# Kernel tuning notes

Hardware: AMD Instinct MI355X
Metric: run time of the kernel (lower is better)

## Reference

```python
import jax, jax.numpy as jnp
import numpy as np
from jax.scipy.special import gammaln

N_L, N_Q, D_IN, D_CTX, H, MAX_AGENT = 256, 65536, 384, 192, 64, 6
STD2 = 0.1
VAR2 = STD2 * STD2
LOG_VAR2 = float(np.log(VAR2))
TEMP = 1.0


def _linear_init(k, out_dim, in_dim):
    k1, k2 = jax.random.split(k)
    s = 1.0 / np.sqrt(in_dim)
    w = jax.random.uniform(k1, (out_dim, in_dim), minval=-s, maxval=s, dtype=jnp.float32)
    b = jax.random.uniform(k2, (out_dim,), minval=-s, maxval=s, dtype=jnp.float32)
    return w, b


def setup_inputs() -> dict:
    key = jax.random.key(0)
    ks = jax.random.split(key, 12)
    fc1_w, fc1_b = _linear_init(ks[0], H, D_IN)
    fc21_w, fc21_b = _linear_init(ks[1], H, H)
    fc22_w, fc22_b = _linear_init(ks[2], H, H)
    fc3_w, fc3_b = _linear_init(ks[3], H, H)
    fc4_w, fc4_b = _linear_init(ks[4], D_IN, H)
    ctx_w, ctx_b = _linear_init(ks[5], H, D_CTX)
    llms = jax.random.normal(ks[6], (N_L, D_IN), dtype=jnp.float32)
    contexts = jax.random.normal(ks[7], (N_Q, D_CTX), dtype=jnp.float32)
    agent_num_int = jax.random.randint(ks[8], (N_Q, 1), 1, MAX_AGENT + 1, dtype=jnp.int32)
    agent_num_float = agent_num_int.astype(jnp.float32)
    noise_eps = jax.random.normal(ks[9], (N_L, H), dtype=jnp.float32)   # VAE reparameterize eps
    rand_u = jax.random.uniform(ks[10], (MAX_AGENT, N_Q, 1), dtype=jnp.float32)  # per-step uniforms
    return dict(llms=llms, contexts=contexts, agent_num_int=agent_num_int,
                agent_num_float=agent_num_float,
                fc1_w=fc1_w, fc1_b=fc1_b, fc21_w=fc21_w, fc21_b=fc21_b,
                fc22_w=fc22_w, fc22_b=fc22_b, fc3_w=fc3_w, fc3_b=fc3_b,
                fc4_w=fc4_w, fc4_b=fc4_b, ctx_w=ctx_w, ctx_b=ctx_b,
                noise_eps=noise_eps, rand_u=rand_u)


def _l2norm(x):
    n = jnp.sqrt(jnp.sum(x * x, axis=1, keepdims=True))
    return x / jnp.maximum(n, 1e-12)


def reference(llms, contexts, agent_num_int, agent_num_float,
              fc1_w, fc1_b, fc21_w, fc21_b, fc22_w, fc22_b,
              fc3_w, fc3_b, fc4_w, fc4_b, ctx_w, ctx_b, noise_eps, rand_u):
    # ---- VAE encode / reparameterize / decode ----
    h = jax.nn.relu(llms @ fc1_w.T + fc1_b)
    mu = h @ fc21_w.T + fc21_b
    log_var = h @ fc22_w.T + fc22_b
    std = jnp.exp(0.5 * log_var) * STD2
    z = mu + noise_eps * std
    h2 = jax.nn.relu(z @ fc3_w.T + fc3_b)
    x_hat = h2 @ fc4_w.T + fc4_b
    mse = jnp.mean((x_hat - llms) ** 2)
    kld = -0.5 * jnp.mean(1.0 - LOG_VAR2 + log_var - (mu ** 2 + jnp.exp(log_var)) / VAR2)
    vae_loss = mse + kld

    # ---- embeddings and routing scores ----
    llm_emb = _l2norm(z)                                   # [N_l, H]
    ctx_emb = _l2norm(contexts @ ctx_w.T + ctx_b)          # [N_q, H]
    scores = jax.nn.softmax((ctx_emb @ llm_emb.T) / TEMP, axis=1)  # [N_q, N_l]
    scores_cumsum = jnp.cumsum(scores, axis=1)

    # ---- vectorized max_agent-step categorical sampling ----
    # sel[i, q] = first llm where cumsum > u (inverse-CDF sampling), for step i
    sel = jnp.argmax(scores_cumsum[None, :, :] > rand_u, axis=2)          # [A, N_q]
    steps = jnp.arange(1, rand_u.shape[0] + 1, dtype=agent_num_int.dtype)
    mask = (agent_num_int[None, :, 0] >= steps[:, None]).astype(scores.dtype)  # [A, N_q]
    rows = jnp.broadcast_to(jnp.arange(scores.shape[0])[None, :], sel.shape)
    selected_llm = jnp.zeros_like(scores).at[rows, sel].add(mask)          # [N_q, N_l]

    log_probs = (gammaln(agent_num_float + 1.0)
                 - jnp.sum(gammaln(selected_llm + 1.0), axis=1, keepdims=True)
                 + jnp.sum(selected_llm * jnp.log(scores), axis=1, keepdims=True))
    return selected_llm, log_probs, vae_loss
```

## Files before the change

kernel.cpp:

```cpp
#include <hip/hip_runtime.h>
#include <hip/hip_bf16.h>

#define N_L 256
#define N_Q 65536
#define D_IN 384
#define D_CTX 192
#define HDIM 64
#define MAXA 6

__device__ __forceinline__ void fma4(float& acc, const float4& w, const float4& v) {
    acc = fmaf(w.x, v.x, acc);
    acc = fmaf(w.y, v.y, acc);
    acc = fmaf(w.z, v.z, acc);
    acc = fmaf(w.w, v.w, acc);
}

__device__ __forceinline__ float lgfact(int n) {
    return (n <= 1) ? 0.0f :
           (n == 2) ? 0.6931471805599453f :
           (n == 3) ? 1.7917594692280550f :
           (n == 4) ? 3.1780538303479458f :
           (n == 5) ? 4.7874917427820460f :
                      6.5792512120101010f;
}

__global__ __launch_bounds__(64) void vae_kernel(
    const float* __restrict__ llms, const float* __restrict__ ctx_w,
    const float* __restrict__ fc1_w, const float* __restrict__ fc1_b,
    const float* __restrict__ fc21_w, const float* __restrict__ fc21_b,
    const float* __restrict__ fc22_w, const float* __restrict__ fc22_b,
    const float* __restrict__ fc3_w, const float* __restrict__ fc3_b,
    const float* __restrict__ fc4_w, const float* __restrict__ fc4_b,
    const float* __restrict__ eps,
    float* __restrict__ ctx_wP, float* __restrict__ embT,
    float* __restrict__ mse_row, float* __restrict__ kld_row)
{
    __shared__ __align__(16) float xs[D_IN];
    __shared__ __align__(16) float hs[HDIM];
    __shared__ __align__(16) float zs[HDIM];
    __shared__ __align__(16) float h2s[HDIM];
    const int r = blockIdx.x;
    const int j = threadIdx.x;

    {
        int f = r * 64 + j;
        if (f < D_CTX * HDIM) {
            int p = f >> 2, rr = f & 3;
            int jc = p & 63, k4 = p >> 6;
            ctx_wP[f] = ctx_w[jc * D_CTX + k4 * 4 + rr];
        }
    }

    for (int k = j; k < D_IN; k += 64) xs[k] = llms[r * D_IN + k];
    __syncthreads();

    float acc = fc1_b[j];
    {
        const float4* wr = (const float4*)(fc1_w + (size_t)j * D_IN);
        const float4* xr = (const float4*)xs;
        #pragma unroll 8
        for (int k4 = 0; k4 < D_IN / 4; ++k4) { fma4(acc, wr[k4], xr[k4]); }
    }
    float h = fmaxf(acc, 0.0f);
    hs[j] = h;
    __syncthreads();

    float mu = fc21_b[j], lv = fc22_b[j];
    {
        const float4* w1 = (const float4*)(fc21_w + (size_t)j * HDIM);
        const float4* w2 = (const float4*)(fc22_w + (size_t)j * HDIM);
        const float4* hr = (const float4*)hs;
        #pragma unroll
        for (int k4 = 0; k4 < HDIM / 4; ++k4) {
            float4 hh = hr[k4];
            fma4(mu, w1[k4], hh);
            fma4(lv, w2[k4], hh);
        }
    }
    float stdv = expf(0.5f * lv) * 0.1f;
    float z = fmaf(eps[r * HDIM + j], stdv, mu);

    float elv = expf(lv);
    float kt = (1.0f - (-4.60517018598809136f)) + lv - (mu * mu + elv) / 0.01f;
    float ks = kt;
    #pragma unroll
    for (int o = 32; o; o >>= 1) ks += __shfl_xor(ks, o);

    float zsq = z * z;
    #pragma unroll
    for (int o = 32; o; o >>= 1) zsq += __shfl_xor(zsq, o);
    float nrm = fmaxf(sqrtf(zsq), 1e-12f);
    embT[j * N_L + r] = z / nrm;
    zs[j] = z;
    __syncthreads();

    float a3 = fc3_b[j];
    {
        const float4* w3 = (const float4*)(fc3_w + (size_t)j * HDIM);
        const float4* zr = (const float4*)zs;
        #pragma unroll
        for (int k4 = 0; k4 < HDIM / 4; ++k4) { fma4(a3, w3[k4], zr[k4]); }
    }
    float h2 = fmaxf(a3, 0.0f);
    h2s[j] = h2;
    __syncthreads();

    float ms = 0.0f;
    const float4* h2r = (const float4*)h2s;
    #pragma unroll
    for (int m = 0; m < 6; ++m) {
        int o = j + 64 * m;
        float a4 = fc4_b[o];
        const float4* w4 = (const float4*)(fc4_w + (size_t)o * HDIM);
        #pragma unroll
        for (int k4 = 0; k4 < HDIM / 4; ++k4) { fma4(a4, w4[k4], h2r[k4]); }
        float d = a4 - xs[o];
        ms = fmaf(d, d, ms);
    }
    #pragma unroll
    for (int o = 32; o; o >>= 1) ms += __shfl_xor(ms, o);
    if (j == 0) { mse_row[r] = ms; kld_row[r] = ks; }
}

__global__ __launch_bounds__(256) void route_kernel(
    const float* __restrict__ contexts, const float* __restrict__ ctx_wP, const float* __restrict__ ctx_b,
    const float* __restrict__ embT, const int* __restrict__ agent_num, const float* __restrict__ rand_u,
    const float* __restrict__ mse_row, const float* __restrict__ kld_row,
    float* __restrict__ out_sel, float* __restrict__ out_lp, float* __restrict__ out_loss)
{
    __shared__ __align__(16) float lds[4][1600];

    const int tid = threadIdx.x;
    const int lane = tid & 63;
    const int widx = tid >> 6;
    const int l0 = lane << 2;

    const int g = blockIdx.x * 4 + widx;
    const int q0 = __builtin_amdgcn_readfirstlane(g << 3);
    float* myl = lds[widx];

    {
        float4* xls = (float4*)myl;
        const float4* cbase = (const float4*)contexts + (size_t)q0 * (D_CTX / 4);
        #pragma unroll
        for (int it = 0; it < 6; ++it) {
            int f = lane + it * 64;
            xls[f] = cbase[f];
        }
        if (lane < 48)
            myl[1536 + lane] = rand_u[(lane >> 3) * N_Q + q0 + (lane & 7)];
    }

    if (g == 0) {
        int rr = lane * 4;
        float ms = mse_row[rr] + mse_row[rr + 1] + mse_row[rr + 2] + mse_row[rr + 3];
        float ks = kld_row[rr] + kld_row[rr + 1] + kld_row[rr + 2] + kld_row[rr + 3];
        #pragma unroll
        for (int o = 32; o; o >>= 1) { ms += __shfl_xor(ms, o); ks += __shfl_xor(ks, o); }
        if (lane == 0) out_loss[0] = ms / 98304.0f - 0.5f * (ks / 16384.0f);
    }

    int Aq[8];
    #pragma unroll
    for (int q = 0; q < 8; ++q)
        Aq[q] = __builtin_amdgcn_readfirstlane(agent_num[q0 + q]);

    const float bj = ctx_b[lane];
    float e[8];
    #pragma unroll
    for (int q = 0; q < 8; ++q) e[q] = bj;
    {
        const float4* wp = (const float4*)ctx_wP;
        const float4* xls = (const float4*)myl;
        #pragma unroll 2
        for (int k4 = 0; k4 < D_CTX / 4; ++k4) {
            float4 w = wp[k4 * HDIM + lane];
            #pragma unroll
            for (int q = 0; q < 8; ++q) {
                float4 xv = xls[q * 48 + k4];
                e[q] = fmaf(w.x, xv.x, e[q]);
                e[q] = fmaf(w.y, xv.y, e[q]);
                e[q] = fmaf(w.z, xv.z, e[q]);
                e[q] = fmaf(w.w, xv.w, e[q]);
            }
        }
    }
    {
        float s[8];
        #pragma unroll
        for (int q = 0; q < 8; ++q) s[q] = e[q] * e[q];
        #pragma unroll
        for (int o = 32; o; o >>= 1)
            #pragma unroll
            for (int q = 0; q < 8; ++q) s[q] += __shfl_xor(s[q], o);
        #pragma unroll
        for (int q = 0; q < 8; ++q) {
            e[q] *= 1.0f / fmaxf(sqrtf(s[q]), 1e-12f);
            myl[q * HDIM + lane] = e[q];
        }
    }

    float4 P[8];
    #pragma unroll
    for (int q = 0; q < 8; ++q) P[q] = make_float4(0.f, 0.f, 0.f, 0.f);

    #pragma unroll 2
    for (int j4 = 0; j4 < HDIM / 4; ++j4) {
        float4 M0 = *(const float4*)(embT + (size_t)(j4 * 4 + 0) * N_L + l0);
        float4 M1 = *(const float4*)(embT + (size_t)(j4 * 4 + 1) * N_L + l0);
        float4 M2 = *(const float4*)(embT + (size_t)(j4 * 4 + 2) * N_L + l0);
        float4 M3 = *(const float4*)(embT + (size_t)(j4 * 4 + 3) * N_L + l0);
        #pragma unroll
        for (int q = 0; q < 8; ++q) {
            float4 ev = *(const float4*)(myl + q * HDIM + j4 * 4);
            P[q].x = fmaf(M0.x, ev.x, P[q].x); P[q].x = fmaf(M1.x, ev.y, P[q].x);
            P[q].x = fmaf(M2.x, ev.z, P[q].x); P[q].x = fmaf(M3.x, ev.w, P[q].x);
            P[q].y = fmaf(M0.y, ev.x, P[q].y); P[q].y = fmaf(M1.y, ev.y, P[q].y);
            P[q].y = fmaf(M2.y, ev.z, P[q].y); P[q].y = fmaf(M3.y, ev.w, P[q].y);
            P[q].z = fmaf(M0.z, ev.x, P[q].z); P[q].z = fmaf(M1.z, ev.y, P[q].z);
            P[q].z = fmaf(M2.z, ev.z, P[q].z); P[q].z = fmaf(M3.z, ev.w, P[q].z);
            P[q].w = fmaf(M0.w, ev.x, P[q].w); P[q].w = fmaf(M1.w, ev.y, P[q].w);
            P[q].w = fmaf(M2.w, ev.z, P[q].w); P[q].w = fmaf(M3.w, ev.w, P[q].w);
        }
    }

    {
        float m[8], s[8];
        #pragma unroll
        for (int k = 0; k < 8; ++k) m[k] = fmaxf(fmaxf(P[k].x, P[k].y), fmaxf(P[k].z, P[k].w));
        #pragma unroll
        for (int o = 32; o; o >>= 1)
            #pragma unroll
            for (int k = 0; k < 8; ++k) m[k] = fmaxf(m[k], __shfl_xor(m[k], o));
        #pragma unroll
        for (int k = 0; k < 8; ++k) {
            P[k].x = expf(P[k].x - m[k]); P[k].y = expf(P[k].y - m[k]);
            P[k].z = expf(P[k].z - m[k]); P[k].w = expf(P[k].w - m[k]);
            s[k] = P[k].x + P[k].y + P[k].z + P[k].w;
        }
        #pragma unroll
        for (int o = 32; o; o >>= 1)
            #pragma unroll
            for (int k = 0; k < 8; ++k) s[k] += __shfl_xor(s[k], o);
        #pragma unroll
        for (int k = 0; k < 8; ++k) {
            float inv = 1.0f / s[k];
            P[k].x *= inv; P[k].y *= inv; P[k].z *= inv; P[k].w *= inv;
        }
    }

    float c0[8], c1[8], c2[8], c3[8];
    {
        float p3[8], t[8];
        #pragma unroll
        for (int k = 0; k < 8; ++k) {
            c0[k] = P[k].x; c1[k] = c0[k] + P[k].y; c2[k] = c1[k] + P[k].z; p3[k] = c2[k] + P[k].w;
            t[k] = p3[k];
        }
        #pragma unroll
        for (int o = 1; o < 64; o <<= 1)
            #pragma unroll
            for (int k = 0; k < 8; ++k) { float v = __shfl_up(t[k], o); if (lane >= o) t[k] += v; }
        #pragma unroll
        for (int k = 0; k < 8; ++k) {
            float base = t[k] - p3[k];
            c0[k] += base; c1[k] += base; c2[k] += base; c3[k] = p3[k] + base;
        }
    }

    unsigned nib[8] = {0, 0, 0, 0, 0, 0, 0, 0};
    #pragma unroll
    for (int i = 0; i < MAXA; ++i) {
        #pragma unroll
        for (int k = 0; k < 8; ++k) {
            if (i < Aq[k]) {
                float u = myl[1536 + i * 8 + k];
                unsigned long long b0 = __ballot(c0[k] <= u);
                unsigned long long b1 = __ballot(c1[k] <= u);
                unsigned long long b2 = __ballot(c2[k] <= u);
                unsigned long long b3 = __ballot(c3[k] <= u);
                int loc = __popcll(b0) + __popcll(b1) + __popcll(b2) + __popcll(b3);
                int sel = (loc >= N_L) ? 0 : loc;
                unsigned d = (unsigned)(sel - l0);
                if (d < 4u) nib[k] += 1u << (4 * d);
            }
        }
    }

    float term[8];
    #pragma unroll
    for (int k = 0; k < 8; ++k) {
        int n0 = nib[k] & 15, n1 = (nib[k] >> 4) & 15, n2 = (nib[k] >> 8) & 15, n3 = (nib[k] >> 12) & 15;
        float4 rowv = make_float4((float)n0, (float)n1, (float)n2, (float)n3);
        *(((float4*)(out_sel + (size_t)(q0 + k) * N_L)) + lane) = rowv;
        float tm = 0.0f;
        if (n0) tm += (float)n0 * logf(P[k].x) - lgfact(n0);
        if (n1) tm += (float)n1 * logf(P[k].y) - lgfact(n1);
        if (n2) tm += (float)n2 * logf(P[k].z) - lgfact(n2);
        if (n3) tm += (float)n3 * logf(P[k].w) - lgfact(n3);
        term[k] = tm;
    }
    #pragma unroll
    for (int o = 32; o; o >>= 1)
        #pragma unroll
        for (int k = 0; k < 8; ++k) term[k] += __shfl_xor(term[k], o);

    if (lane < 8) {
        float rr = term[0];
        int Aa = Aq[0];
        #pragma unroll
        for (int k = 1; k < 8; ++k) {
            if (lane == k) { rr = term[k]; Aa = Aq[k]; }
        }
        out_lp[q0 + lane] = lgfact(Aa) + rr;
    }
}

extern "C" void kernel_launch(void* const* d_in, const int* in_sizes, int n_in,
                              void* d_out, int out_size, void* d_ws, size_t ws_size,
                              hipStream_t stream) {
    const float* llms      = (const float*)d_in[0];
    const float* contexts  = (const float*)d_in[1];
    const int*   agent_i   = (const int*)  d_in[2];
    const float* fc1_w  = (const float*)d_in[4];  const float* fc1_b  = (const float*)d_in[5];
    const float* fc21_w = (const float*)d_in[6];  const float* fc21_b = (const float*)d_in[7];
    const float* fc22_w = (const float*)d_in[8];  const float* fc22_b = (const float*)d_in[9];
    const float* fc3_w  = (const float*)d_in[10]; const float* fc3_b  = (const float*)d_in[11];
    const float* fc4_w  = (const float*)d_in[12]; const float* fc4_b  = (const float*)d_in[13];
    const float* ctx_w  = (const float*)d_in[14]; const float* ctx_b  = (const float*)d_in[15];
    const float* noise  = (const float*)d_in[16]; const float* rand_u = (const float*)d_in[17];

    float* out      = (float*)d_out;
    float* out_sel  = out;
    float* out_lp   = out + (size_t)N_Q * N_L;
    float* out_loss = out_lp + N_Q;

    float* ctx_wP   = (float*)d_ws;
    float* embT     = ctx_wP + D_CTX * HDIM;
    float* mse_row  = embT + HDIM * N_L;
    float* kld_row  = mse_row + N_L;

    vae_kernel<<<N_L, 64, 0, stream>>>(llms, ctx_w, fc1_w, fc1_b, fc21_w, fc21_b, fc22_w, fc22_b,
                                       fc3_w, fc3_b, fc4_w, fc4_b, noise,
                                       ctx_wP, embT, mse_row, kld_row);
    route_kernel<<<2048, 256, 0, stream>>>(contexts, ctx_wP, ctx_b, embT, agent_i, rand_u,
                                           mse_row, kld_row, out_sel, out_lp, out_loss);
}
```

Measured before the change: 228.6 us.

## Move VAE decoder into extra route-kernel blocks and halve route LDS

Splits the VAE kernel so the small serial pre-kernel only runs the encoder. The fc3/fc4 decoder and MSE run as 64 extra blocks appended to the route kernel, with an atomic accumulator and a last-arriver counter to finalize the loss. The route kernel also stages contexts into LDS in two halves, which cuts per-wave LDS from 1600 to 832 floats, and sets launch_bounds to 8 blocks so occupancy can rise. The risks are atomic nondeterminism in the MSE sum and added register pressure from the occupancy hint.

```diff
diff --git a/kernel.cpp b/kernel.cpp
--- a/kernel.cpp
+++ b/kernel.cpp
@@ -7,6 +7,8 @@
 #define D_CTX 192
 #define HDIM 64
 #define MAXA 6
+#define NBLK_ROUTE 2048
+#define NBLK_DEC 64
 
 __device__ __forceinline__ void fma4(float& acc, const float4& w, const float4& v) {
     acc = fmaf(w.x, v.x, acc);
@@ -24,23 +26,21 @@
                       6.5792512120101010f;
 }
 
-__global__ __launch_bounds__(64) void vae_kernel(
+__global__ __launch_bounds__(64) void enc_kernel(
     const float* __restrict__ llms, const float* __restrict__ ctx_w,
     const float* __restrict__ fc1_w, const float* __restrict__ fc1_b,
     const float* __restrict__ fc21_w, const float* __restrict__ fc21_b,
     const float* __restrict__ fc22_w, const float* __restrict__ fc22_b,
-    const float* __restrict__ fc3_w, const float* __restrict__ fc3_b,
-    const float* __restrict__ fc4_w, const float* __restrict__ fc4_b,
     const float* __restrict__ eps,
-    float* __restrict__ ctx_wP, float* __restrict__ embT,
-    float* __restrict__ mse_row, float* __restrict__ kld_row)
+    float* __restrict__ ctx_wP, float* __restrict__ embT, float* __restrict__ z_ws,
+    float* __restrict__ kld_row, float* __restrict__ acc, int* __restrict__ counter)
 {
     __shared__ __align__(16) float xs[D_IN];
     __shared__ __align__(16) float hs[HDIM];
-    __shared__ __align__(16) float zs[HDIM];
-    __shared__ __align__(16) float h2s[HDIM];
     const int r = blockIdx.x;
     const int j = threadIdx.x;
+
+    if (r == 0 && j == 0) { acc[0] = 0.0f; counter[0] = 0; }
 
     {
         int f = r * 64 + j;
@@ -54,14 +54,14 @@
     for (int k = j; k < D_IN; k += 64) xs[k] = llms[r * D_IN + k];
     __syncthreads();
 
-    float acc = fc1_b[j];
+    float acc1 = fc1_b[j];
     {
         const float4* wr = (const float4*)(fc1_w + (size_t)j * D_IN);
         const float4* xr = (const float4*)xs;
         #pragma unroll 8
-        for (int k4 = 0; k4 < D_IN / 4; ++k4) { fma4(acc, wr[k4], xr[k4]); }
-    }
-    float h = fmaxf(acc, 0.0f);
+        for (int k4 = 0; k4 < D_IN / 4; ++k4) { fma4(acc1, wr[k4], xr[k4]); }
+    }
+    float h = fmaxf(acc1, 0.0f);
     hs[j] = h;
     __syncthreads();
 
@@ -79,6 +79,7 @@
     }
     float stdv = expf(0.5f * lv) * 0.1f;
     float z = fmaf(eps[r * HDIM + j], stdv, mu);
+    z_ws[r * HDIM + j] = z;
 
     float elv = expf(lv);
     float kt = (1.0f - (-4.60517018598809136f)) + lv - (mu * mu + elv) / 0.01f;
@@ -91,74 +92,78 @@
     for (int o = 32; o; o >>= 1) zsq += __shfl_xor(zsq, o);
     float nrm = fmaxf(sqrtf(zsq), 1e-12f);
     embT[j * N_L + r] = z / nrm;
-    zs[j] = z;
-    __syncthreads();
-
-    float a3 = fc3_b[j];
-    {
-        const float4* w3 = (const float4*)(fc3_w + (size_t)j * HDIM);
-        const float4* zr = (const float4*)zs;
-        #pragma unroll
-        for (int k4 = 0; k4 < HDIM / 4; ++k4) { fma4(a3, w3[k4], zr[k4]); }
-    }
-    float h2 = fmaxf(a3, 0.0f);
-    h2s[j] = h2;
-    __syncthreads();
-
-    float ms = 0.0f;
-    const float4* h2r = (const float4*)h2s;
-    #pragma unroll
-    for (int m = 0; m < 6; ++m) {
-        int o = j + 64 * m;
-        float a4 = fc4_b[o];
-        const float4* w4 = (const float4*)(fc4_w + (size_t)o * HDIM);
-        #pragma unroll
-        for (int k4 = 0; k4 < HDIM / 4; ++k4) { fma4(a4, w4[k4], h2r[k4]); }
-        float d = a4 - xs[o];
-        ms = fmaf(d, d, ms);
-    }
-    #pragma unroll
-    for (int o = 32; o; o >>= 1) ms += __shfl_xor(ms, o);
-    if (j == 0) { mse_row[r] = ms; kld_row[r] = ks; }
-}
-
-__global__ __launch_bounds__(256) void route_kernel(
+
+    if (j == 0) kld_row[r] = ks;
+}
+
+__global__ __launch_bounds__(256, 8) void route_kernel(
     const float* __restrict__ contexts, const float* __restrict__ ctx_wP, const float* __restrict__ ctx_b,
     const float* __restrict__ embT, const int* __restrict__ agent_num, const float* __restrict__ rand_u,
-    const float* __restrict__ mse_row, const float* __restrict__ kld_row,
+    const float* __restrict__ z_ws, const float* __restrict__ llms,
+    const float* __restrict__ fc3_w, const float* __restrict__ fc3_b,
+    const float* __restrict__ fc4_w, const float* __restrict__ fc4_b,
+    const float* __restrict__ kld_row, float* __restrict__ acc, int* __restrict__ counter,
     float* __restrict__ out_sel, float* __restrict__ out_lp, float* __restrict__ out_loss)
 {
-    __shared__ __align__(16) float lds[4][1600];
+    __shared__ __align__(16) float lds[4][832];
 
     const int tid = threadIdx.x;
     const int lane = tid & 63;
     const int widx = tid >> 6;
+    float* myl = lds[widx];
+
+    if (blockIdx.x >= NBLK_ROUTE) {
+        const int r = (blockIdx.x - NBLK_ROUTE) * 4 + widx;
+        myl[lane] = z_ws[r * HDIM + lane];
+        float a3 = fc3_b[lane];
+        {
+            const float4* w3 = (const float4*)(fc3_w + (size_t)lane * HDIM);
+            const float4* zr = (const float4*)myl;
+            #pragma unroll
+            for (int k4 = 0; k4 < HDIM / 4; ++k4) { fma4(a3, w3[k4], zr[k4]); }
+        }
+        myl[HDIM + lane] = fmaxf(a3, 0.0f);
+        float ms = 0.0f;
+        const float4* h2r = (const float4*)(myl + HDIM);
+        #pragma unroll
+        for (int m = 0; m < 6; ++m) {
+            int o = lane + 64 * m;
+            float a4 = fc4_b[o];
+            const float4* w4 = (const float4*)(fc4_w + (size_t)o * HDIM);
+            #pragma unroll
+            for (int k4 = 0; k4 < HDIM / 4; ++k4) { fma4(a4, w4[k4], h2r[k4]); }
+            float d = a4 - llms[r * D_IN + o];
+            ms = fmaf(d, d, ms);
+        }
+        #pragma unroll
+        for (int o = 32; o; o >>= 1) ms += __shfl_xor(ms, o);
+
+        int old = 0;
+        if (lane == 0) {
+            atomicAdd(acc, ms);
+            __threadfence();
+            old = atomicAdd(counter, 1);
+        }
+        old = __shfl(old, 0);
+        if (old == N_L - 1) {
+            float ks = kld_row[lane * 4] + kld_row[lane * 4 + 1]
+                     + kld_row[lane * 4 + 2] + kld_row[lane * 4 + 3];
+            #pragma unroll
+            for (int o = 32; o; o >>= 1) ks += __shfl_xor(ks, o);
+            if (lane == 0) {
+                float mtot = atomicAdd(acc, 0.0f);
+                out_loss[0] = mtot / 98304.0f - 0.5f * (ks / 16384.0f);
+            }
+        }
+        return;
+    }
+
     const int l0 = lane << 2;
-
     const int g = blockIdx.x * 4 + widx;
     const int q0 = __builtin_amdgcn_readfirstlane(g << 3);
-    float* myl = lds[widx];
-
-    {
-        float4* xls = (float4*)myl;
-        const float4* cbase = (const float4*)contexts + (size_t)q0 * (D_CTX / 4);
-        #pragma unroll
-        for (int it = 0; it < 6; ++it) {
-            int f = lane + it * 64;
-            xls[f] = cbase[f];
-        }
-        if (lane < 48)
-            myl[1536 + lane] = rand_u[(lane >> 3) * N_Q + q0 + (lane & 7)];
-    }
-
-    if (g == 0) {
-        int rr = lane * 4;
-        float ms = mse_row[rr] + mse_row[rr + 1] + mse_row[rr + 2] + mse_row[rr + 3];
-        float ks = kld_row[rr] + kld_row[rr + 1] + kld_row[rr + 2] + kld_row[rr + 3];
-        #pragma unroll
-        for (int o = 32; o; o >>= 1) { ms += __shfl_xor(ms, o); ks += __shfl_xor(ks, o); }
-        if (lane == 0) out_loss[0] = ms / 98304.0f - 0.5f * (ks / 16384.0f);
-    }
+
+    if (lane < 48)
+        myl[768 + lane] = rand_u[(lane >> 3) * N_Q + q0 + (lane & 7)];
 
     int Aq[8];
     #pragma unroll
@@ -171,17 +176,28 @@
     for (int q = 0; q < 8; ++q) e[q] = bj;
     {
         const float4* wp = (const float4*)ctx_wP;
-        const float4* xls = (const float4*)myl;
-        #pragma unroll 2
-        for (int k4 = 0; k4 < D_CTX / 4; ++k4) {
-            float4 w = wp[k4 * HDIM + lane];
-            #pragma unroll
-            for (int q = 0; q < 8; ++q) {
-                float4 xv = xls[q * 48 + k4];
-                e[q] = fmaf(w.x, xv.x, e[q]);
-                e[q] = fmaf(w.y, xv.y, e[q]);
-                e[q] = fmaf(w.z, xv.z, e[q]);
-                e[q] = fmaf(w.w, xv.w, e[q]);
+        const float4* cbase = (const float4*)contexts + (size_t)q0 * (D_CTX / 4);
+        float4* xls = (float4*)myl;
+        #pragma unroll
+        for (int hh = 0; hh < 2; ++hh) {
+            #pragma unroll
+            for (int it = 0; it < 3; ++it) {
+                int f = lane + it * 64;
+                int q = f / 24, kk = f - q * 24;
+                xls[f] = cbase[q * 48 + hh * 24 + kk];
+            }
+            #pragma unroll 2
+            for (int kk = 0; kk < 24; ++kk) {
+                int k4 = hh * 24 + kk;
+                float4 w = wp[k4 * HDIM + lane];
+                #pragma unroll
+                for (int q = 0; q < 8; ++q) {
+                    float4 xv = xls[q * 24 + kk];
+                    e[q] = fmaf(w.x, xv.x, e[q]);
+                    e[q] = fmaf(w.y, xv.y, e[q]);
+                    e[q] = fmaf(w.z, xv.z, e[q]);
+                    e[q] = fmaf(w.w, xv.w, e[q]);
+                }
             }
         }
     }
@@ -274,7 +290,7 @@
         #pragma unroll
         for (int k = 0; k < 8; ++k) {
             if (i < Aq[k]) {
-                float u = myl[1536 + i * 8 + k];
+                float u = myl[768 + i * 8 + k];
                 unsigned long long b0 = __ballot(c0[k] <= u);
                 unsigned long long b1 = __ballot(c1[k] <= u);
                 unsigned long long b2 = __ballot(c2[k] <= u);
@@ -337,12 +353,16 @@
 
     float* ctx_wP   = (float*)d_ws;
     float* embT     = ctx_wP + D_CTX * HDIM;
-    float* mse_row  = embT + HDIM * N_L;
-    float* kld_row  = mse_row + N_L;
-
-    vae_kernel<<<N_L, 64, 0, stream>>>(llms, ctx_w, fc1_w, fc1_b, fc21_w, fc21_b, fc22_w, fc22_b,
-                                       fc3_w, fc3_b, fc4_w, fc4_b, noise,
-                                       ctx_wP, embT, mse_row, kld_row);
-    route_kernel<<<2048, 256, 0, stream>>>(contexts, ctx_wP, ctx_b, embT, agent_i, rand_u,
-                                           mse_row, kld_row, out_sel, out_lp, out_loss);
-}
+    float* z_ws     = embT + HDIM * N_L;
+    float* kld_row  = z_ws + N_L * HDIM;
+    float* acc      = kld_row + N_L;
+    int*   counter  = (int*)(acc + 1);
+
+    enc_kernel<<<N_L, 64, 0, stream>>>(llms, ctx_w, fc1_w, fc1_b, fc21_w, fc21_b,
+                                       fc22_w, fc22_b, noise,
+                                       ctx_wP, embT, z_ws, kld_row, acc, counter);
+    route_kernel<<<NBLK_ROUTE + NBLK_DEC, 256, 0, stream>>>(
+        contexts, ctx_wP, ctx_b, embT, agent_i, rand_u,
+        z_ws, llms, fc3_w, fc3_b, fc4_w, fc4_b, kld_row, acc, counter,
+        out_sel, out_lp, out_loss);
+}
```

After: 457.1 us. +100.0%, slower.
